# Performance work log

Hardware: AMD Instinct MI355X
Metric: run time of the kernel (lower is better)

Reference implementation:

```python
import jax, jax.numpy as jnp
import numpy as np
import math

NUM_CLASSES = 100000
EMBED = 384
BATCH = 512
S = 64.0
M = 0.5
COS_M = math.cos(M)
SIN_M = math.sin(M)
TH = math.cos(math.pi - M)
MM = math.sin(math.pi - M) * M
EPS = 1e-07


def setup_inputs() -> dict:
    key = jax.random.key(0)
    k1, k2, k3 = jax.random.split(key, 3)
    embeddings = jax.random.normal(k1, (BATCH, EMBED), dtype=jnp.float32)
    labels = jax.random.randint(k2, (BATCH,), 0, NUM_CLASSES, dtype=jnp.int64)
    # xavier_uniform-like init for weight [num_classes, embedding_size]
    limit = math.sqrt(6.0 / (NUM_CLASSES + EMBED))
    weight = jax.random.uniform(k3, (NUM_CLASSES, EMBED), dtype=jnp.float32,
                                minval=-limit, maxval=limit)
    return {"embeddings": embeddings, "labels": labels, "weight": weight}


def reference(embeddings, labels, weight):
    # normalize class weights (note: embeddings are NOT normalized, per source)
    W = weight / jnp.linalg.norm(weight, axis=1, keepdims=True)  # [C, E]
    cos_theta = jnp.clip(embeddings @ W.T, -1.0 + EPS, 1.0 - EPS)  # [B, C]
    sin_theta = jnp.sqrt(1.0 - cos_theta ** 2)
    cos_theta_m = cos_theta * COS_M - sin_theta * SIN_M
    cos_theta_m = jnp.where(cos_theta > TH, cos_theta_m, cos_theta - MM)
    one_hot = jax.nn.one_hot(labels, cos_theta.shape[1], dtype=cos_theta.dtype)
    logits = S * (one_hot * cos_theta_m + (1.0 - one_hot) * cos_theta)
    # mean cross-entropy
    logp = jax.nn.log_softmax(logits, axis=-1)  # [B, C]
    nll = -jnp.take_along_axis(logp, labels[:, None], axis=1)[:, 0]
    return jnp.mean(nll)
```

## Files before the change

### kernel.cpp

```cpp
#include <hip/hip_runtime.h>
#include <hip/hip_bf16.h>
#include <math.h>

#define C_CLASSES 100000
#define EMBED     384
#define BATCH     512
#define S_SCALE   64.0f
#define COS_M_    0.8775825618903728f
#define SIN_M_    0.479425538604203f
#define TH_       (-0.8775825618903728f)
#define MM_       0.2397127693021015f
#define EPS_      1e-7f
#define LOG2E_    1.4426950408889634f
#define LN2_      0.6931471805599453f
#define BIGZ_     92.33261191693459f
#define SK1_      92.33248f

#define CT    64
#define NCH   1563

typedef __attribute__((ext_vector_type(8))) short bf16x8;
typedef __attribute__((ext_vector_type(4))) float f32x4;

__device__ inline ushort f2bf(float f) {
    unsigned u = __float_as_uint(f);
    unsigned r = (u + 0x7fffu + ((u >> 16) & 1u)) >> 16;
    return (ushort)r;
}

__global__ __launch_bounds__(256)
void cvt_pack_e(const float* __restrict__ emb, ushort* __restrict__ eP)
{
    int t = blockIdx.x * 256 + threadIdx.x;
    int lane = t & 63;
    int grp  = t >> 6;
    int tile = grp / 12, ks = grp % 12;
    int lr = lane & 15, lg = lane >> 4;
    int row = tile * 16 + lr;
    int col = ks * 32 + lg * 8;
    const float4* src = (const float4*)(emb + (size_t)row * EMBED + col);
    float4 v0 = src[0], v1 = src[1];
    ushort4 o0, o1;
    o0.x = f2bf(v0.x); o0.y = f2bf(v0.y); o0.z = f2bf(v0.z); o0.w = f2bf(v0.w);
    o1.x = f2bf(v1.x); o1.y = f2bf(v1.y); o1.z = f2bf(v1.z); o1.w = f2bf(v1.w);
    ((ushort4*)eP)[t * 2]     = o0;
    ((ushort4*)eP)[t * 2 + 1] = o1;
}

__global__ __launch_bounds__(512, 4)
void arc_fused64(const ushort* __restrict__ eP, const int* __restrict__ labels,
                 const float* __restrict__ weight,
                 float* __restrict__ psum, float* __restrict__ zlabel)
{
    __shared__ ushort Bl[(CT / 16) * 12 * 512];
    __shared__ int    labL[BATCH];

    const int tid = threadIdx.x;

    const int orig = blockIdx.x;
    const int xcd  = orig & 7;
    const int qq   = NCH >> 3, rr = NCH & 7;
    const int blk  = (xcd < rr ? xcd * (qq + 1)
                               : rr * (qq + 1) + (xcd - rr) * qq) + (orig >> 3);
    const int c0   = blk * CT;

    labL[tid] = labels[tid];

    {
        const int p = tid & 15;
        #pragma unroll
        for (int h = 0; h < 2; ++h) {
            const int c = h * 32 + (tid >> 4);
            int row = c0 + c;
            if (row >= C_CLASSES) row = C_CLASSES - 1;
            const float4* src = (const float4*)(weight + (size_t)row * EMBED) + p;

            float4 wv[6];
            float ss = 0.f;
            #pragma unroll
            for (int i = 0; i < 6; ++i) {
                wv[i] = src[16 * i];
                ss += wv[i].x * wv[i].x + wv[i].y * wv[i].y
                    + wv[i].z * wv[i].z + wv[i].w * wv[i].w;
            }
            ss += __shfl_xor(ss, 1, 64);
            ss += __shfl_xor(ss, 2, 64);
            ss += __shfl_xor(ss, 4, 64);
            ss += __shfl_xor(ss, 8, 64);
            const float inv = (ss > 0.f) ? rsqrtf(ss) : 0.f;

            const int t2 = c >> 4, cl = c & 15;
            #pragma unroll
            for (int i = 0; i < 6; ++i) {
                int q   = p + 16 * i;
                int ks  = q >> 3;
                int lgp = (q >> 1) & 3;
                int jo  = (q & 1) * 4;
                ushort4 o;
                o.x = f2bf(wv[i].x * inv); o.y = f2bf(wv[i].y * inv);
                o.z = f2bf(wv[i].z * inv); o.w = f2bf(wv[i].w * inv);
                *(ushort4*)&Bl[(size_t)(((t2 * 12 + ks) * 64) + cl + 16 * lgp) * 8 + jo] = o;
            }
        }
    }
    __syncthreads();

    const int wid = tid >> 6, l = tid & 63;
    const int lr  = l & 15,  lg = l >> 4;

    const ushort* abase = eP + ((size_t)(wid * 4) * 12 * 64 + l) * 8;

    f32x4 acc[4][4];
    #pragma unroll
    for (int mt = 0; mt < 4; ++mt)
        #pragma unroll
        for (int nt = 0; nt < 4; ++nt)
            acc[mt][nt] = (f32x4){0.f, 0.f, 0.f, 0.f};

    #pragma unroll
    for (int ks = 0; ks < 12; ++ks) {
        bf16x8 a[4], b[4];
        #pragma unroll
        for (int mt = 0; mt < 4; ++mt)
            a[mt] = *(const bf16x8*)(abase + (mt * 12 + ks) * 512);
        #pragma unroll
        for (int nt = 0; nt < 4; ++nt)
            b[nt] = *(const bf16x8*)&Bl[(size_t)((nt * 12 + ks) * 64 + l) * 8];
        #pragma unroll
        for (int mt = 0; mt < 4; ++mt)
            #pragma unroll
            for (int nt = 0; nt < 4; ++nt)
                acc[mt][nt] = __builtin_amdgcn_mfma_f32_16x16x32_bf16(
                    a[mt], b[nt], acc[mt][nt], 0, 0, 0);
    }

    const bool tail = (blk == NCH - 1);
    #pragma unroll
    for (int mt = 0; mt < 4; ++mt) {
        #pragma unroll
        for (int rg = 0; rg < 4; ++rg) {
            const int r   = wid * 64 + mt * 16 + lg * 4 + rg;
            const int lab = labL[r];
            float acc4 = 0.f;
            if (!tail) {
                #pragma unroll
                for (int nt = 0; nt < 4; ++nt) {
                    float cv = acc[mt][nt][rg];
                    cv = fminf(fmaxf(cv, -1.f + EPS_), 1.f - EPS_);
                    acc4 += exp2f(fmaf(cv, SK1_, -BIGZ_));
                }
            } else {
                #pragma unroll
                for (int nt = 0; nt < 4; ++nt) {
                    float cv = acc[mt][nt][rg];
                    cv = fminf(fmaxf(cv, -1.f + EPS_), 1.f - EPS_);
                    float z = fmaf(cv, SK1_, -BIGZ_);
                    int gc = c0 + nt * 16 + lr;
                    if (gc >= C_CLASSES) z = -1e30f;
                    acc4 += exp2f(z);
                }
            }
            int off = lab - c0;
            if (((unsigned)off < 64u) && ((off & 15) == lr)) {
                int ntl = off >> 4;
                float cv = (ntl == 0) ? acc[mt][0][rg]
                         : (ntl == 1) ? acc[mt][1][rg]
                         : (ntl == 2) ? acc[mt][2][rg]
                                      : acc[mt][3][rg];
                cv = fminf(fmaxf(cv, -1.f + EPS_), 1.f - EPS_);
                float plain = exp2f(fmaf(cv, SK1_, -BIGZ_));
                float zm;
                if (cv > TH_) {
                    float sv = sqrtf(fmaxf(1.f - cv * cv, 0.f));
                    zm = S_SCALE * (cv * COS_M_ - sv * SIN_M_);
                } else {
                    zm = S_SCALE * (cv - MM_);
                }
                acc4 += exp2f(fmaf(zm, LOG2E_, -BIGZ_)) - plain;
                zlabel[r] = zm;
            }
            acc4 += __shfl_xor(acc4, 1, 64);
            acc4 += __shfl_xor(acc4, 2, 64);
            acc4 += __shfl_xor(acc4, 4, 64);
            acc4 += __shfl_xor(acc4, 8, 64);
            if (lr == 0) psum[(size_t)blk * BATCH + r] = acc4;
        }
    }
}

__global__ __launch_bounds__(256)
void arc_reduce(const float* __restrict__ psum, const float* __restrict__ zlabel,
                float* __restrict__ rowloss)
{
    const int r = blockIdx.x;
    const int tid = threadIdx.x;
    float s = 0.f;
    for (int k = tid; k < NCH; k += 256)
        s += psum[(size_t)k * BATCH + r];
    #pragma unroll
    for (int d = 1; d < 64; d <<= 1) s += __shfl_xor(s, d, 64);
    __shared__ float ssh[4];
    if ((tid & 63) == 0) ssh[tid >> 6] = s;
    __syncthreads();
    if (tid == 0) {
        float t = ssh[0] + ssh[1] + ssh[2] + ssh[3];
        rowloss[r] = LN2_ * (BIGZ_ + log2f(t)) - zlabel[r];
    }
}

__global__ __launch_bounds__(512)
void arc_mean(const float* __restrict__ rowloss, float* __restrict__ out)
{
    const int tid = threadIdx.x;
    float v = rowloss[tid];
    #pragma unroll
    for (int d = 1; d < 64; d <<= 1) v += __shfl_xor(v, d, 64);
    __shared__ float sv[8];
    if ((tid & 63) == 0) sv[tid >> 6] = v;
    __syncthreads();
    if (tid == 0) {
        float t = 0.f;
        #pragma unroll
        for (int w = 0; w < 8; ++w) t += sv[w];
        out[0] = t / (float)BATCH;
    }
}

extern "C" void kernel_launch(void* const* d_in, const int* in_sizes, int n_in,
                              void* d_out, int out_size, void* d_ws, size_t ws_size,
                              hipStream_t stream)
{
    (void)in_sizes; (void)n_in; (void)out_size; (void)ws_size;
    const float* emb    = (const float*)d_in[0];
    const int*   labels = (const int*)d_in[1];
    const float* weight = (const float*)d_in[2];
    float* out = (float*)d_out;

    float*  psum    = (float*)d_ws;
    float*  zlabel  = psum + (size_t)NCH * BATCH;
    float*  rowloss = zlabel + BATCH;
    ushort* eP      = (ushort*)(rowloss + BATCH);

    cvt_pack_e<<<(BATCH * EMBED / 8) / 256, 256, 0, stream>>>(emb, eP);
    arc_fused64<<<NCH, 512, 0, stream>>>(eP, labels, weight, psum, zlabel);
    arc_reduce<<<BATCH, 256, 0, stream>>>(psum, zlabel, rowloss);
    arc_mean<<<1, 512, 0, stream>>>(rowloss, out);
}
```

Baseline: 99.91 us.

## Use persistent producer/consumer blocks with double-buffered weight staging

Replaces the one-block-per-chunk kernel with 256 persistent blocks of 12 waves. Four producer waves load, normalize and bf16-pack the next 64-class weight chunk into a second LDS buffer while eight consumer waves run MFMA and the softmax partial sums on the current chunk. The goal is to hide global-load latency behind compute. In exchange, only 256 blocks run (about one per CU), producers do no math, and there is a block-wide barrier every iteration, so overlap may be limited.

```diff
diff --git a/kernel.cpp b/kernel.cpp
--- a/kernel.cpp
+++ b/kernel.cpp
@@ -18,6 +18,7 @@
 
 #define CT    64
 #define NCH   1563
+#define NB    256
 
 typedef __attribute__((ext_vector_type(8))) short bf16x8;
 typedef __attribute__((ext_vector_type(4))) float f32x4;
@@ -47,145 +48,157 @@
     ((ushort4*)eP)[t * 2 + 1] = o1;
 }
 
-__global__ __launch_bounds__(512, 4)
-void arc_fused64(const ushort* __restrict__ eP, const int* __restrict__ labels,
-                 const float* __restrict__ weight,
-                 float* __restrict__ psum, float* __restrict__ zlabel)
-{
-    __shared__ ushort Bl[(CT / 16) * 12 * 512];
+__global__ __launch_bounds__(768, 3)
+void arc_pc(const ushort* __restrict__ eP, const int* __restrict__ labels,
+            const float* __restrict__ weight,
+            float* __restrict__ psum, float* __restrict__ zlabel)
+{
+    __shared__ ushort Bl[2][(CT / 16) * 12 * 512];
     __shared__ int    labL[BATCH];
 
     const int tid = threadIdx.x;
-
-    const int orig = blockIdx.x;
-    const int xcd  = orig & 7;
-    const int qq   = NCH >> 3, rr = NCH & 7;
-    const int blk  = (xcd < rr ? xcd * (qq + 1)
-                               : rr * (qq + 1) + (xcd - rr) * qq) + (orig >> 3);
-    const int c0   = blk * CT;
-
-    labL[tid] = labels[tid];
-
-    {
-        const int p = tid & 15;
-        #pragma unroll
-        for (int h = 0; h < 2; ++h) {
-            const int c = h * 32 + (tid >> 4);
-            int row = c0 + c;
-            if (row >= C_CLASSES) row = C_CLASSES - 1;
-            const float4* src = (const float4*)(weight + (size_t)row * EMBED) + p;
-
-            float4 wv[6];
-            float ss = 0.f;
+    const int blk = blockIdx.x;
+    const int nch = 6 + ((blk < (NCH - 6 * NB)) ? 1 : 0);
+
+    if (tid < BATCH) labL[tid] = labels[tid];
+
+    const int wid = tid >> 6;
+    const bool producer = (wid < 4);
+
+#define STAGE(CH, BUF) do {                                                   \
+        const int p_ = tid & 7;                                               \
+        _Pragma("unroll")                                                     \
+        for (int h_ = 0; h_ < 2; ++h_) {                                      \
+            const int c_ = h_ * 32 + (tid >> 3);                   \
+            int row_ = (CH) * CT + c_;                                        \
+            if (row_ >= C_CLASSES) row_ = C_CLASSES - 1;                      \
+            const float4* s_ =                                                \
+                (const float4*)(weight + (size_t)row_ * EMBED) + p_;          \
+            float4 wv_[12];                                                   \
+            float ss_ = 0.f;                                                  \
+            _Pragma("unroll")                                                 \
+            for (int i_ = 0; i_ < 12; ++i_) {                                 \
+                wv_[i_] = s_[8 * i_];                                         \
+                ss_ += wv_[i_].x * wv_[i_].x + wv_[i_].y * wv_[i_].y          \
+                     + wv_[i_].z * wv_[i_].z + wv_[i_].w * wv_[i_].w;         \
+            }                                                                 \
+            ss_ += __shfl_xor(ss_, 1, 64);                                    \
+            ss_ += __shfl_xor(ss_, 2, 64);                                    \
+            ss_ += __shfl_xor(ss_, 4, 64);                                    \
+            const float inv_ = (ss_ > 0.f) ? rsqrtf(ss_) : 0.f;               \
+            const int t2_ = c_ >> 4, cl_ = c_ & 15;                           \
+            _Pragma("unroll")                                                 \
+            for (int i_ = 0; i_ < 12; ++i_) {                                 \
+                int q_   = p_ + 8 * i_;                                       \
+                int ks_  = q_ >> 3;                                           \
+                int lgp_ = (q_ >> 1) & 3;                                     \
+                int jo_  = (q_ & 1) * 4;                                      \
+                ushort4 o_;                                                   \
+                o_.x = f2bf(wv_[i_].x * inv_); o_.y = f2bf(wv_[i_].y * inv_); \
+                o_.z = f2bf(wv_[i_].z * inv_); o_.w = f2bf(wv_[i_].w * inv_); \
+                *(ushort4*)&Bl[BUF][(size_t)(((t2_ * 12 + ks_) * 64)          \
+                        + cl_ + 16 * lgp_) * 8 + jo_] = o_;                   \
+            }                                                                 \
+        }                                                                     \
+    } while (0)
+
+    const int cw = wid - 4;
+    const int l  = tid & 63;
+    const int lr = l & 15, lg = l >> 4;
+    const ushort* abase = eP + ((size_t)(cw * 4) * 12 * 64 + l) * 8;
+
+    if (producer) STAGE(blk, 0);
+    __syncthreads();
+
+    int ch = blk;
+    for (int k = 0; k < nch; ++k) {
+        const int cur = k & 1;
+        if (producer) {
+            if (k + 1 < nch) STAGE(ch + NB, cur ^ 1);
+        } else {
+            const int  c0   = ch * CT;
+            const bool tail = (ch == NCH - 1);
+
+            f32x4 acc[4][4];
             #pragma unroll
-            for (int i = 0; i < 6; ++i) {
-                wv[i] = src[16 * i];
-                ss += wv[i].x * wv[i].x + wv[i].y * wv[i].y
-                    + wv[i].z * wv[i].z + wv[i].w * wv[i].w;
+            for (int mt = 0; mt < 4; ++mt)
+                #pragma unroll
+                for (int nt = 0; nt < 4; ++nt)
+                    acc[mt][nt] = (f32x4){0.f, 0.f, 0.f, 0.f};
+
+            #pragma unroll
+            for (int ks = 0; ks < 12; ++ks) {
+                bf16x8 a[4], b[4];
+                #pragma unroll
+                for (int mt = 0; mt < 4; ++mt)
+                    a[mt] = *(const bf16x8*)(abase + (mt * 12 + ks) * 512);
+                #pragma unroll
+                for (int nt = 0; nt < 4; ++nt)
+                    b[nt] = *(const bf16x8*)&Bl[cur][(size_t)((nt * 12 + ks) * 64 + l) * 8];
+                #pragma unroll
+                for (int mt = 0; mt < 4; ++mt)
+                    #pragma unroll
+                    for (int nt = 0; nt < 4; ++nt)
+                        acc[mt][nt] = __builtin_amdgcn_mfma_f32_16x16x32_bf16(
+                            a[mt], b[nt], acc[mt][nt], 0, 0, 0);
             }
-            ss += __shfl_xor(ss, 1, 64);
-            ss += __shfl_xor(ss, 2, 64);
-            ss += __shfl_xor(ss, 4, 64);
-            ss += __shfl_xor(ss, 8, 64);
-            const float inv = (ss > 0.f) ? rsqrtf(ss) : 0.f;
-
-            const int t2 = c >> 4, cl = c & 15;
+
             #pragma unroll
-            for (int i = 0; i < 6; ++i) {
-                int q   = p + 16 * i;
-                int ks  = q >> 3;
-                int lgp = (q >> 1) & 3;
-                int jo  = (q & 1) * 4;
-                ushort4 o;
-                o.x = f2bf(wv[i].x * inv); o.y = f2bf(wv[i].y * inv);
-                o.z = f2bf(wv[i].z * inv); o.w = f2bf(wv[i].w * inv);
-                *(ushort4*)&Bl[(size_t)(((t2 * 12 + ks) * 64) + cl + 16 * lgp) * 8 + jo] = o;
+            for (int mt = 0; mt < 4; ++mt) {
+                #pragma unroll
+                for (int rg = 0; rg < 4; ++rg) {
+                    const int r   = cw * 64 + mt * 16 + lg * 4 + rg;
+                    const int lab = labL[r];
+                    float acc4 = 0.f;
+                    if (!tail) {
+                        #pragma unroll
+                        for (int nt = 0; nt < 4; ++nt) {
+                            float cv = acc[mt][nt][rg];
+                            cv = fminf(fmaxf(cv, -1.f + EPS_), 1.f - EPS_);
+                            acc4 += exp2f(fmaf(cv, SK1_, -BIGZ_));
+                        }
+                    } else {
+                        #pragma unroll
+                        for (int nt = 0; nt < 4; ++nt) {
+                            float cv = acc[mt][nt][rg];
+                            cv = fminf(fmaxf(cv, -1.f + EPS_), 1.f - EPS_);
+                            float z = fmaf(cv, SK1_, -BIGZ_);
+                            int gc = c0 + nt * 16 + lr;
+                            if (gc >= C_CLASSES) z = -1e30f;
+                            acc4 += exp2f(z);
+                        }
+                    }
+                    int off = lab - c0;
+                    if (((unsigned)off < 64u) && ((off & 15) == lr)) {
+                        int ntl = off >> 4;
+                        float cv = (ntl == 0) ? acc[mt][0][rg]
+                                 : (ntl == 1) ? acc[mt][1][rg]
+                                 : (ntl == 2) ? acc[mt][2][rg]
+                                              : acc[mt][3][rg];
+                        cv = fminf(fmaxf(cv, -1.f + EPS_), 1.f - EPS_);
+                        float plain = exp2f(fmaf(cv, SK1_, -BIGZ_));
+                        float zm;
+                        if (cv > TH_) {
+                            float sv = sqrtf(fmaxf(1.f - cv * cv, 0.f));
+                            zm = S_SCALE * (cv * COS_M_ - sv * SIN_M_);
+                        } else {
+                            zm = S_SCALE * (cv - MM_);
+                        }
+                        acc4 += exp2f(fmaf(zm, LOG2E_, -BIGZ_)) - plain;
+                        zlabel[r] = zm;
+                    }
+                    acc4 += __shfl_xor(acc4, 1, 64);
+                    acc4 += __shfl_xor(acc4, 2, 64);
+                    acc4 += __shfl_xor(acc4, 4, 64);
+                    acc4 += __shfl_xor(acc4, 8, 64);
+                    if (lr == 0) psum[(size_t)ch * BATCH + r] = acc4;
+                }
             }
         }
+        __syncthreads();
+        ch += NB;
     }
-    __syncthreads();
-
-    const int wid = tid >> 6, l = tid & 63;
-    const int lr  = l & 15,  lg = l >> 4;
-
-    const ushort* abase = eP + ((size_t)(wid * 4) * 12 * 64 + l) * 8;
-
-    f32x4 acc[4][4];
-    #pragma unroll
-    for (int mt = 0; mt < 4; ++mt)
-        #pragma unroll
-        for (int nt = 0; nt < 4; ++nt)
-            acc[mt][nt] = (f32x4){0.f, 0.f, 0.f, 0.f};
-
-    #pragma unroll
-    for (int ks = 0; ks < 12; ++ks) {
-        bf16x8 a[4], b[4];
-        #pragma unroll
-        for (int mt = 0; mt < 4; ++mt)
-            a[mt] = *(const bf16x8*)(abase + (mt * 12 + ks) * 512);
-        #pragma unroll
-        for (int nt = 0; nt < 4; ++nt)
-            b[nt] = *(const bf16x8*)&Bl[(size_t)((nt * 12 + ks) * 64 + l) * 8];
-        #pragma unroll
-        for (int mt = 0; mt < 4; ++mt)
-            #pragma unroll
-            for (int nt = 0; nt < 4; ++nt)
-                acc[mt][nt] = __builtin_amdgcn_mfma_f32_16x16x32_bf16(
-                    a[mt], b[nt], acc[mt][nt], 0, 0, 0);
-    }
-
-    const bool tail = (blk == NCH - 1);
-    #pragma unroll
-    for (int mt = 0; mt < 4; ++mt) {
-        #pragma unroll
-        for (int rg = 0; rg < 4; ++rg) {
-            const int r   = wid * 64 + mt * 16 + lg * 4 + rg;
-            const int lab = labL[r];
-            float acc4 = 0.f;
-            if (!tail) {
-                #pragma unroll
-                for (int nt = 0; nt < 4; ++nt) {
-                    float cv = acc[mt][nt][rg];
-                    cv = fminf(fmaxf(cv, -1.f + EPS_), 1.f - EPS_);
-                    acc4 += exp2f(fmaf(cv, SK1_, -BIGZ_));
-                }
-            } else {
-                #pragma unroll
-                for (int nt = 0; nt < 4; ++nt) {
-                    float cv = acc[mt][nt][rg];
-                    cv = fminf(fmaxf(cv, -1.f + EPS_), 1.f - EPS_);
-                    float z = fmaf(cv, SK1_, -BIGZ_);
-                    int gc = c0 + nt * 16 + lr;
-                    if (gc >= C_CLASSES) z = -1e30f;
-                    acc4 += exp2f(z);
-                }
-            }
-            int off = lab - c0;
-            if (((unsigned)off < 64u) && ((off & 15) == lr)) {
-                int ntl = off >> 4;
-                float cv = (ntl == 0) ? acc[mt][0][rg]
-                         : (ntl == 1) ? acc[mt][1][rg]
-                         : (ntl == 2) ? acc[mt][2][rg]
-                                      : acc[mt][3][rg];
-                cv = fminf(fmaxf(cv, -1.f + EPS_), 1.f - EPS_);
-                float plain = exp2f(fmaf(cv, SK1_, -BIGZ_));
-                float zm;
-                if (cv > TH_) {
-                    float sv = sqrtf(fmaxf(1.f - cv * cv, 0.f));
-                    zm = S_SCALE * (cv * COS_M_ - sv * SIN_M_);
-                } else {
-                    zm = S_SCALE * (cv - MM_);
-                }
-                acc4 += exp2f(fmaf(zm, LOG2E_, -BIGZ_)) - plain;
-                zlabel[r] = zm;
-            }
-            acc4 += __shfl_xor(acc4, 1, 64);
-            acc4 += __shfl_xor(acc4, 2, 64);
-            acc4 += __shfl_xor(acc4, 4, 64);
-            acc4 += __shfl_xor(acc4, 8, 64);
-            if (lr == 0) psum[(size_t)blk * BATCH + r] = acc4;
-        }
-    }
+#undef STAGE
 }
 
 __global__ __launch_bounds__(256)
@@ -242,7 +255,7 @@
     ushort* eP      = (ushort*)(rowloss + BATCH);
 
     cvt_pack_e<<<(BATCH * EMBED / 8) / 256, 256, 0, stream>>>(emb, eP);
-    arc_fused64<<<NCH, 512, 0, stream>>>(eP, labels, weight, psum, zlabel);
+    arc_pc<<<NB, 768, 0, stream>>>(eP, labels, weight, psum, zlabel);
     arc_reduce<<<BATCH, 256, 0, stream>>>(psum, zlabel, rowloss);
     arc_mean<<<1, 512, 0, stream>>>(rowloss, out);
 }
```

After: 186.0 us. 1.86x slower.

## Stream weights directly from global into MFMA operands with precomputed row norms

Applied to the files above, without the earlier changes.

Moves the weight row-norm computation into a separate pre-pass kernel that writes inverse norms to workspace. The main kernel then drops the shared-memory staging tile and its barrier, and instead has every wave load fp32 weight slices from global memory, scale them and convert them to bf16 right before each MFMA. The aim is to remove the LDS write/sync phase and overlap weight loading with compute. In exchange the full weight matrix is read twice, once by the norm kernel and once by the main kernel. Within a block, each of the 8 waves also reloads and reconverts the same 64 rows, which multiplies cache traffic and conversion work.

```diff
diff --git a/kernel.cpp b/kernel.cpp
--- a/kernel.cpp
+++ b/kernel.cpp
@@ -26,6 +26,11 @@
     unsigned u = __float_as_uint(f);
     unsigned r = (u + 0x7fffu + ((u >> 16) & 1u)) >> 16;
     return (ushort)r;
+}
+
+__device__ inline short cvt_bf(float f) {
+    __hip_bfloat16 h = __float2bfloat16(f);
+    return *(short*)&h;
 }
 
 __global__ __launch_bounds__(256)
@@ -47,13 +52,31 @@
     ((ushort4*)eP)[t * 2 + 1] = o1;
 }
 
+__global__ __launch_bounds__(256)
+void w_norms(const float* __restrict__ weight, float* __restrict__ invn)
+{
+    const int row = blockIdx.x * 16 + (threadIdx.x >> 4);
+    const int p   = threadIdx.x & 15;
+    const float4* src = (const float4*)(weight + (size_t)row * EMBED) + p;
+    float ss = 0.f;
+    #pragma unroll
+    for (int i = 0; i < 6; ++i) {
+        float4 v = src[16 * i];
+        ss += v.x * v.x + v.y * v.y + v.z * v.z + v.w * v.w;
+    }
+    ss += __shfl_xor(ss, 1, 64);
+    ss += __shfl_xor(ss, 2, 64);
+    ss += __shfl_xor(ss, 4, 64);
+    ss += __shfl_xor(ss, 8, 64);
+    if (p == 0) invn[row] = (ss > 0.f) ? rsqrtf(ss) : 0.f;
+}
+
 __global__ __launch_bounds__(512, 4)
-void arc_fused64(const ushort* __restrict__ eP, const int* __restrict__ labels,
-                 const float* __restrict__ weight,
-                 float* __restrict__ psum, float* __restrict__ zlabel)
-{
-    __shared__ ushort Bl[(CT / 16) * 12 * 512];
-    __shared__ int    labL[BATCH];
+void arc_stream(const ushort* __restrict__ eP, const int* __restrict__ labels,
+                const float* __restrict__ weight, const float* __restrict__ invn,
+                float* __restrict__ psum, float* __restrict__ zlabel)
+{
+    __shared__ int labL[BATCH];
 
     const int tid = threadIdx.x;
 
@@ -66,50 +89,21 @@
 
     labL[tid] = labels[tid];
 
-    {
-        const int p = tid & 15;
-        #pragma unroll
-        for (int h = 0; h < 2; ++h) {
-            const int c = h * 32 + (tid >> 4);
-            int row = c0 + c;
-            if (row >= C_CLASSES) row = C_CLASSES - 1;
-            const float4* src = (const float4*)(weight + (size_t)row * EMBED) + p;
-
-            float4 wv[6];
-            float ss = 0.f;
-            #pragma unroll
-            for (int i = 0; i < 6; ++i) {
-                wv[i] = src[16 * i];
-                ss += wv[i].x * wv[i].x + wv[i].y * wv[i].y
-                    + wv[i].z * wv[i].z + wv[i].w * wv[i].w;
-            }
-            ss += __shfl_xor(ss, 1, 64);
-            ss += __shfl_xor(ss, 2, 64);
-            ss += __shfl_xor(ss, 4, 64);
-            ss += __shfl_xor(ss, 8, 64);
-            const float inv = (ss > 0.f) ? rsqrtf(ss) : 0.f;
-
-            const int t2 = c >> 4, cl = c & 15;
-            #pragma unroll
-            for (int i = 0; i < 6; ++i) {
-                int q   = p + 16 * i;
-                int ks  = q >> 3;
-                int lgp = (q >> 1) & 3;
-                int jo  = (q & 1) * 4;
-                ushort4 o;
-                o.x = f2bf(wv[i].x * inv); o.y = f2bf(wv[i].y * inv);
-                o.z = f2bf(wv[i].z * inv); o.w = f2bf(wv[i].w * inv);
-                *(ushort4*)&Bl[(size_t)(((t2 * 12 + ks) * 64) + cl + 16 * lgp) * 8 + jo] = o;
-            }
-        }
-    }
-    __syncthreads();
-
     const int wid = tid >> 6, l = tid & 63;
     const int lr  = l & 15,  lg = l >> 4;
 
     const ushort* abase = eP + ((size_t)(wid * 4) * 12 * 64 + l) * 8;
 
+    const float* wrow[4];
+    float binv[4];
+    #pragma unroll
+    for (int nt = 0; nt < 4; ++nt) {
+        int gc = c0 + nt * 16 + lr;
+        if (gc >= C_CLASSES) gc = C_CLASSES - 1;
+        wrow[nt] = weight + (size_t)gc * EMBED + lg * 8;
+        binv[nt] = invn[gc];
+    }
+
     f32x4 acc[4][4];
     #pragma unroll
     for (int mt = 0; mt < 4; ++mt)
@@ -119,19 +113,25 @@
 
     #pragma unroll
     for (int ks = 0; ks < 12; ++ks) {
-        bf16x8 a[4], b[4];
+        bf16x8 a[4];
         #pragma unroll
         for (int mt = 0; mt < 4; ++mt)
             a[mt] = *(const bf16x8*)(abase + (mt * 12 + ks) * 512);
         #pragma unroll
-        for (int nt = 0; nt < 4; ++nt)
-            b[nt] = *(const bf16x8*)&Bl[(size_t)((nt * 12 + ks) * 64 + l) * 8];
-        #pragma unroll
-        for (int mt = 0; mt < 4; ++mt)
+        for (int nt = 0; nt < 4; ++nt) {
+            const float4* wp = (const float4*)(wrow[nt] + ks * 32);
+            float4 w0 = wp[0], w1 = wp[1];
+            const float iv = binv[nt];
+            bf16x8 b;
+            b[0] = cvt_bf(w0.x * iv); b[1] = cvt_bf(w0.y * iv);
+            b[2] = cvt_bf(w0.z * iv); b[3] = cvt_bf(w0.w * iv);
+            b[4] = cvt_bf(w1.x * iv); b[5] = cvt_bf(w1.y * iv);
+            b[6] = cvt_bf(w1.z * iv); b[7] = cvt_bf(w1.w * iv);
             #pragma unroll
-            for (int nt = 0; nt < 4; ++nt)
+            for (int mt = 0; mt < 4; ++mt)
                 acc[mt][nt] = __builtin_amdgcn_mfma_f32_16x16x32_bf16(
-                    a[mt], b[nt], acc[mt][nt], 0, 0, 0);
+                    a[mt], b, acc[mt][nt], 0, 0, 0);
+        }
     }
 
     const bool tail = (blk == NCH - 1);
@@ -239,10 +239,12 @@
     float*  psum    = (float*)d_ws;
     float*  zlabel  = psum + (size_t)NCH * BATCH;
     float*  rowloss = zlabel + BATCH;
-    ushort* eP      = (ushort*)(rowloss + BATCH);
+    float*  invn    = rowloss + BATCH;
+    ushort* eP      = (ushort*)(invn + C_CLASSES);
 
     cvt_pack_e<<<(BATCH * EMBED / 8) / 256, 256, 0, stream>>>(emb, eP);
-    arc_fused64<<<NCH, 512, 0, stream>>>(eP, labels, weight, psum, zlabel);
+    w_norms<<<C_CLASSES / 16, 256, 0, stream>>>(weight, invn);
+    arc_stream<<<NCH, 512, 0, stream>>>(eP, labels, weight, invn, psum, zlabel);
     arc_reduce<<<BATCH, 256, 0, stream>>>(psum, zlabel, rowloss);
     arc_mean<<<1, 512, 0, stream>>>(rowloss, out);
 }
```

After: 228.9 us. +129.1%, slower.
